# Kernel optimization log

Hardware: AMD Instinct MI355X
Metric: run time of the kernel (lower is better)

The kernel has to match this reference:

```python
import jax, jax.numpy as jnp
import numpy as np

NH = 2  # attention heads


def _mha(q, k, v, w, b, pool):
    """2-head attention; w:[4,D,D] (q,k,v,o as x@W), b:[4,D], pool:[Lq] pools query axis -> [B,D]."""
    B, Lq, D = q.shape
    dk = D // NH
    Q = (q @ w[0] + b[0]).reshape(B, Lq, NH, dk).transpose(0, 2, 1, 3)
    K = (k @ w[1] + b[1]).reshape(B, -1, NH, dk).transpose(0, 2, 1, 3)
    V = (v @ w[2] + b[2]).reshape(B, -1, NH, dk).transpose(0, 2, 1, 3)
    scores = jnp.einsum('bhqd,bhkd->bhqk', Q, K) / jnp.sqrt(jnp.asarray(dk, q.dtype))
    attn = jax.nn.softmax(scores, axis=-1)
    ctx = jnp.einsum('bhqk,bhkd->bqhd', attn, V).reshape(B, Lq, D)
    out = ctx @ w[3] + b[3]              # [B, Lq, D]
    return jnp.einsum('bqd,q->bd', out, pool)  # pooled over query axis (w_size)


def setup_inputs() -> dict:
    key = jax.random.key(0)
    ks = jax.random.split(key, 32)
    B, T, D, N = 64, 32, 768, 901
    s = 0.02
    inp = {
        'question_embeds': jax.random.normal(ks[0], (B, T, D), jnp.float32),
        'image_local_embeds': jax.random.normal(ks[1], (B, N, D), jnp.float32),
        'h0': jax.random.uniform(ks[2], (B, D), jnp.float32),
        'gru_w_ih': jax.random.normal(ks[3], (3 * D, D), jnp.float32) * s,
        'gru_w_hh': jax.random.normal(ks[4], (3 * D, D), jnp.float32) * s,
        'gru_b_ih': jax.random.normal(ks[5], (3 * D,), jnp.float32) * s,
        'gru_b_hh': jax.random.normal(ks[6], (3 * D,), jnp.float32) * s,
        'ga_w': jax.random.normal(ks[7], (4, D, D), jnp.float32) * s,
        'ga_b': jax.random.normal(ks[8], (4, D), jnp.float32) * s,
        'ga_pool': jax.random.normal(ks[9], (1,), jnp.float32),
        'la_w': jax.random.normal(ks[10], (4, D, D), jnp.float32) * s,
        'la_b': jax.random.normal(ks[11], (4, D), jnp.float32) * s,
        'la_pool': jax.random.normal(ks[12], (T,), jnp.float32) * 0.2,
        'go_w': jax.random.normal(ks[13], (4, D, D), jnp.float32) * s,
        'go_b': jax.random.normal(ks[14], (4, D), jnp.float32) * s,
        'go_pool': jax.random.normal(ks[15], (T,), jnp.float32) * 0.2,
        'f1_w': jax.random.normal(ks[16], (2 * D, 1024), jnp.float32) * s,
        'f1_b': jax.random.normal(ks[17], (1024,), jnp.float32) * s,
        'f2_w': jax.random.normal(ks[18], (1024, 512), jnp.float32) * s,
        'f2_b': jax.random.normal(ks[19], (512,), jnp.float32) * s,
        'f3_w': jax.random.normal(ks[20], (512, 1024), jnp.float32) * s,
        'f3_b': jax.random.normal(ks[21], (1024,), jnp.float32) * s,
    }
    return inp


def reference(question_embeds, image_local_embeds, h0,
              gru_w_ih, gru_w_hh, gru_b_ih, gru_b_hh,
              ga_w, ga_b, ga_pool, la_w, la_b, la_pool,
              go_w, go_b, go_pool,
              f1_w, f1_b, f2_w, f2_b, f3_w, f3_b):
    img_cls = image_local_embeds[:, :1, :]        # [B,1,D] global CLS token
    img_loc = image_local_embeds[:, 1:, :]        # [B,N-1,D] patch tokens
    Hs = h0.shape[-1]

    def step(h, x_t):
        # per-timestep cross-attention of question token against image CLS
        a = _mha(x_t[:, None, :], img_cls, img_cls, ga_w, ga_b, ga_pool)  # [B,D]
        wx = a @ gru_w_ih.T                      # [B,3H]
        wh = h @ gru_w_hh.T
        r = jax.nn.sigmoid(wx[:, :Hs] + wh[:, :Hs] + gru_b_ih[:Hs] + gru_b_hh[:Hs])
        z = jax.nn.sigmoid(wx[:, Hs:2 * Hs] + wh[:, Hs:2 * Hs]
                           + gru_b_ih[Hs:2 * Hs] + gru_b_hh[Hs:2 * Hs])
        n = jnp.tanh(wx[:, 2 * Hs:] + gru_b_ih[2 * Hs:]
                     + r * (wh[:, 2 * Hs:] + gru_b_hh[2 * Hs:]))
        h_new = (1 - z) * n + z * h
        return h_new, h_new

    xs = jnp.swapaxes(question_embeds, 0, 1)      # [T,B,D]
    _, ys = jax.lax.scan(step, h0, xs)
    q_emb = jnp.swapaxes(ys, 0, 1)                # [B,T,D]

    local_out = _mha(q_emb, img_loc, img_loc, la_w, la_b, la_pool)   # [B,D]
    gobal_out = _mha(q_emb, img_cls, img_cls, go_w, go_b, go_pool)   # [B,D]
    h = jnp.concatenate([local_out, gobal_out], axis=1)              # [B,2D]
    x = h @ f1_w + f1_b
    x = jax.nn.relu(x @ f2_w + f2_b)
    return x @ f3_w + f3_b                                           # [B,1024]
```

## Files before the change

### kernel.cpp

```cpp
#include <hip/hip_runtime.h>
#include <math.h>


typedef short bf16x8 __attribute__((ext_vector_type(8)));
typedef float f32x4 __attribute__((ext_vector_type(4)));
typedef unsigned short ushort_t;

#define GRU_NB 48

__device__ __forceinline__ unsigned short f2b(float f) {
    unsigned int u = __float_as_uint(f);
    unsigned int r = (u + 0x7FFFu + ((u >> 16) & 1u)) >> 16;
    return (unsigned short)r;
}
__device__ __forceinline__ float b2f(unsigned short s) {
    return __uint_as_float(((unsigned int)s) << 16);
}
__device__ __forceinline__ float sigm(float x) { return 1.f / (1.f + __expf(-x)); }
__device__ __forceinline__ float tanhx(float x) {
    x = fminf(fmaxf(x, -15.f), 15.f);
    float e = __expf(2.f * x);
    return (e - 1.f) / (e + 1.f);
}

__device__ __forceinline__ void gbar(int* flags, int nb, int phase, int bid, int tid) {
    __syncthreads();
    if (tid == 0) __hip_atomic_store(&flags[bid], phase, __ATOMIC_RELAXED, __HIP_MEMORY_SCOPE_AGENT);
    if (tid < 64) {
        for (;;) {
            int v = 0x7fffffff;
            for (int f = tid; f < nb; f += 64)
                v = min(v, __hip_atomic_load(&flags[f], __ATOMIC_RELAXED, __HIP_MEMORY_SCOPE_AGENT));
            if (__all(v >= phase)) break;
            __builtin_amdgcn_s_sleep(1);
        }
    }
    __syncthreads();
}


__global__ void k_cvt_all(const float* __restrict__ whh, const float* __restrict__ la0,
                          const float* __restrict__ la1, const float* __restrict__ h0,
                          const float* __restrict__ gp, const float* __restrict__ lp,
                          ushort_t* __restrict__ whhb, ushort_t* __restrict__ law0b,
                          ushort_t* __restrict__ law1b, ushort_t* __restrict__ h0b,
                          float* __restrict__ hbuf, float* __restrict__ scal,
                          int* __restrict__ bar) {
    if (blockIdx.x == 0) {
        int t = threadIdx.x;
        if (t < 64) {
            float v1 = (t < 32) ? gp[t] : 0.f;
            float v2 = (t < 32) ? lp[t] : 0.f;
#pragma unroll
            for (int m = 1; m < 32; m <<= 1) { v1 += __shfl_xor(v1, m, 64); v2 += __shfl_xor(v2, m, 64); }
            if (t == 0) { scal[0] = v1; scal[1] = v2; }
        }
        for (int i = threadIdx.x; i < 1024; i += 256) bar[i] = 0;
    }
    long i = (long)blockIdx.x * 256 + threadIdx.x;
    const long n1 = 2304L * 768, n2 = n1 + 768L * 768, n3 = n2 + 768L * 768, n4 = n3 + 64L * 768;
    if (i < n1) whhb[i] = f2b(whh[i]);
    else if (i < n2) law0b[i - n1] = f2b(la0[i - n1]);
    else if (i < n3) law1b[i - n2] = f2b(la1[i - n2]);
    else if (i < n4) { float v = h0[i - n3]; h0b[i - n3] = f2b(v); hbuf[i - n3] = v; }
}


template<int MR>
__device__ __forceinline__ void tgemm4(
    const float* __restrict__ A, long lda,
    const float* __restrict__ Bm, int ldb, int transB,
    const float* __restrict__ bias, float s1, float s2,
    const float* __restrict__ bias2, int b2lim,
    float* __restrict__ C, int ldc, int K, int relu, int agent,
    int m0, int n0, float* As, int tid)
{
    for (int r = 0; r < MR; r++)
        for (int k = tid; k < K; k += 256)
            As[r * K + k] = A[(long)(m0 + r) * lda + k];
    __syncthreads();
    int cl = tid & 63, kc = tid >> 6;
    int c = n0 + cl;
    int K4 = K >> 2;
    int kb = kc * K4;
    const float* Bp = transB ? (Bm + (long)c * ldb) : (Bm + c);
    float acc[MR];
#pragma unroll
    for (int r = 0; r < MR; r++) acc[r] = 0.f;
    for (int k = kb; k < kb + K4; k += 8) {
        float bv[8];
        if (!transB) {
#pragma unroll
            for (int i = 0; i < 8; i++) bv[i] = Bp[(long)(k + i) * ldb];
        } else {
            float4 q0 = *(const float4*)(Bp + k);
            float4 q1 = *(const float4*)(Bp + k + 4);
            bv[0] = q0.x; bv[1] = q0.y; bv[2] = q0.z; bv[3] = q0.w;
            bv[4] = q1.x; bv[5] = q1.y; bv[6] = q1.z; bv[7] = q1.w;
        }
#pragma unroll
        for (int i = 0; i < 8; i += 4) {
#pragma unroll
            for (int r = 0; r < MR; r++) {
                float4 x = *(const float4*)&As[r * K + k + i];
                acc[r] += x.x * bv[i] + x.y * bv[i + 1] + x.z * bv[i + 2] + x.w * bv[i + 3];
            }
        }
    }
    __syncthreads();
    float* Red = As;
#pragma unroll
    for (int r = 0; r < MR; r++) Red[(kc * MR + r) * 64 + cl] = acc[r];
    __syncthreads();
    {
        int rg = tid >> 6;
        float bb = (bias ? bias[c] * s2 : 0.f) + ((bias2 && c < b2lim) ? bias2[c] : 0.f);
#pragma unroll
        for (int i = 0; i < MR / 4; i++) {
            int r = rg + i * 4;
            float sum = (Red[(0 * MR + r) * 64 + cl] + Red[(1 * MR + r) * 64 + cl])
                      + (Red[(2 * MR + r) * 64 + cl] + Red[(3 * MR + r) * 64 + cl]);
            float o = sum * s1 + bb;
            if (relu) o = fmaxf(o, 0.f);
            if (agent) __hip_atomic_store(&C[(long)(m0 + r) * ldc + c], o,
                                          __ATOMIC_RELAXED, __HIP_MEMORY_SCOPE_AGENT);
            else C[(long)(m0 + r) * ldc + c] = o;
        }
    }
}


struct HeadP {
    const float *img, *ga_w2, *ga_b2, *go_w2, *go_b2;
    const float *ga_w3, *ga_b3, *go_w3, *go_b3;
    const float *ga_pool, *scal, *w_ih, *b_ih, *b_hh;
    float *t12, *t12g, *avec, *hcat, *base;
    int* flags; int p0, p1;
};

__global__ void __launch_bounds__(256) k_head(HeadP P) {
    __shared__ __align__(16) float As[16 * 768];
    int bid = blockIdx.x, tid = threadIdx.x;
    for (int p = P.p0; p <= P.p1; p++) {
        if (p == 1) {
            if (bid < 192) {
                int prob = bid / 96, r = bid % 96, m8 = r / 12, ct = r % 12;
                tgemm4<8>(P.img, 901L * 768, prob ? P.go_w2 : P.ga_w2, 768, 0,
                          prob ? P.go_b2 : P.ga_b2, 1.f, 1.f, nullptr, 0,
                          prob ? P.t12g : P.t12, 768, 768, 0, 1, m8 * 8, ct * 64, As, tid);
            }
        } else if (p == 2) {
            if (bid < 192) {
                int prob = bid / 96, r = bid % 96, m8 = r / 12, ct = r % 12;
                float sc = prob ? P.scal[0] : P.ga_pool[0];
                tgemm4<8>(prob ? P.t12g : P.t12, 768, prob ? P.go_w3 : P.ga_w3, 768, 0,
                          prob ? P.go_b3 : P.ga_b3, sc, sc, nullptr, 0,
                          prob ? (P.hcat + 768) : P.avec, prob ? 1536 : 768, 768, 0, 1,
                          m8 * 8, ct * 64, As, tid);
            }
        } else if (p == 3) {
            if (bid < 144) {
                int m4 = bid / 36, ct = bid % 36;
                tgemm4<16>(P.avec, 768, P.w_ih, 768, 1, P.b_ih, 1.f, 1.f, P.b_hh, 1536,
                           P.base, 2304, 768, 0, 0, m4 * 16, ct * 64, As, tid);
            }
        }
        if (p < P.p1) gbar(P.flags, 192, p, bid, tid);
    }
}


struct GruP {
    const ushort_t* h0b; const float* h0f; const ushort_t* whh;
    const float* base; const float* bhh; ushort_t* qemb; int* flags;
};

__global__ void __launch_bounds__(384) k_gru_coop(GruP P) {
    __shared__ __align__(16) ushort_t whh_s[3][16][776];
    __shared__ float ps[2][3][64][20];
    __shared__ float bs[3][64][20];
    __shared__ float h_s[64][20];
    __shared__ float bhh_s[16];
    int tid = threadIdx.x;
    int wid = tid >> 6, lane = tid & 63, quad = lane >> 4, l16 = lane & 15;
    int g = wid >> 1, kh = wid & 1;
    int j = blockIdx.x, d0 = j * 16;
    {
        int gS = (wid < 3) ? wid : wid - 3;
        int r0 = (wid < 3) ? 0 : 8;
        for (int r = r0; r < r0 + 8; r++)
            for (int kk = lane * 8; kk < 768; kk += 512)
                *(bf16x8*)&whh_s[gS][r][kk] = *(const bf16x8*)&P.whh[(size_t)(gS * 768 + d0 + r) * 768 + kk];
    }
    for (int e = tid; e < 3072; e += 384) {
        int g2 = e >> 10, rem = e & 1023, b = rem >> 4, c = rem & 15;
        bs[g2][b][c] = P.base[b * 2304 + g2 * 768 + d0 + c];
    }
    for (int e = tid; e < 1024; e += 384) {
        int b = e >> 4, c = e & 15;
        h_s[b][c] = P.h0f[b * 768 + d0 + c];
    }
    if (tid < 16) bhh_s[tid] = P.bhh[1536 + d0 + tid];
    __syncthreads();
    for (int t = 0; t < 32; t++) {
        const ushort_t* Ap = (t == 0) ? P.h0b : (P.qemb + (size_t)(t - 1) * 768);
        size_t ldA = (t == 0) ? 768 : (size_t)32 * 768;
        f32x4 zz4 = {0.f, 0.f, 0.f, 0.f};
        f32x4 acc[4];
#pragma unroll
        for (int mi = 0; mi < 4; mi++) acc[mi] = zz4;
        int kbase = kh * 384;
        for (int kk = kbase; kk < kbase + 384; kk += 32) {
            bf16x8 bfr = *(const bf16x8*)&whh_s[g][l16][kk + quad * 8];
#pragma unroll
            for (int mi = 0; mi < 4; mi++) {
                bf16x8 af = *(const bf16x8*)(Ap + (size_t)(mi * 16 + l16) * ldA + kk + quad * 8);
                acc[mi] = __builtin_amdgcn_mfma_f32_16x16x32_bf16(af, bfr, acc[mi], 0, 0, 0);
            }
        }
#pragma unroll
        for (int mi = 0; mi < 4; mi++)
#pragma unroll
            for (int r = 0; r < 4; r++)
                ps[kh][g][mi * 16 + quad * 4 + r][l16] = acc[mi][r];
        __syncthreads();
        for (int e = tid; e < 512; e += 384) {
            int b = e >> 3, c0 = (e & 7) * 2;
            float hn[2];
#pragma unroll
            for (int u = 0; u < 2; u++) {
                int c = c0 + u;
                float g0 = ps[0][0][b][c] + ps[1][0][b][c];
                float g1 = ps[0][1][b][c] + ps[1][1][b][c];
                float g2v = ps[0][2][b][c] + ps[1][2][b][c];
                float rr = sigm(g0 + bs[0][b][c]);
                float zg = sigm(g1 + bs[1][b][c]);
                float nn = tanhx(bs[2][b][c] + rr * (g2v + bhh_s[c]));
                float hv = h_s[b][c];
                hn[u] = (1.f - zg) * nn + zg * hv;
                h_s[b][c] = hn[u];
            }
            unsigned int pk = (unsigned int)f2b(hn[0]) | ((unsigned int)f2b(hn[1]) << 16);
            __hip_atomic_store((unsigned int*)&P.qemb[((size_t)b * 32 + t) * 768 + d0 + c0],
                               pk, __ATOMIC_RELAXED, __HIP_MEMORY_SCOPE_AGENT);
        }
        __syncthreads();
        if (t < 31) {
            if (tid == 0)
                __hip_atomic_store(&P.flags[j], t + 1, __ATOMIC_RELAXED, __HIP_MEMORY_SCOPE_AGENT);
            if (tid < 64) {
                for (;;) {
                    int v = (tid < GRU_NB)
                        ? __hip_atomic_load(&P.flags[tid], __ATOMIC_RELAXED, __HIP_MEMORY_SCOPE_AGENT)
                        : 0x7fffffff;
                    if (__all(v > t)) break;
                    __builtin_amdgcn_s_sleep(1);
                }
            }
            __syncthreads();
        }
    }
}

__global__ void __launch_bounds__(256) k_gru_step(
    int t, const ushort_t* h0b, const ushort_t* whh, const float* base,
    const float* bhh, float* h, ushort_t* qemb)
{
    int wv = threadIdx.x >> 6, lane = threadIdx.x & 63;
    int quad = lane >> 4, l16 = lane & 15;
    int d0 = blockIdx.x * 64 + wv * 16;
    float bhhn = bhh[1536 + d0 + l16];
    const ushort_t* Ap = (t == 0) ? h0b : (qemb + (long)(t - 1) * 768);
    long ldA = (t == 0) ? 768 : 32 * 768;
    int d = d0 + l16;
    f32x4 zz4 = {0.f, 0.f, 0.f, 0.f};
    f32x4 acc[3][4];
#pragma unroll
    for (int g = 0; g < 3; g++)
#pragma unroll
        for (int mi = 0; mi < 4; mi++) acc[g][mi] = zz4;
    for (int kk = 0; kk < 768; kk += 32) {
        bf16x8 af[4];
#pragma unroll
        for (int mi = 0; mi < 4; mi++)
            af[mi] = *(const bf16x8*)(Ap + (long)(mi * 16 + l16) * ldA + kk + quad * 8);
#pragma unroll
        for (int g = 0; g < 3; g++) {
            bf16x8 bfr = *(const bf16x8*)(whh + (long)(g * 768 + d0 + l16) * 768 + kk + quad * 8);
#pragma unroll
            for (int mi = 0; mi < 4; mi++)
                acc[g][mi] = __builtin_amdgcn_mfma_f32_16x16x32_bf16(af[mi], bfr, acc[g][mi], 0, 0, 0);
        }
    }
#pragma unroll
    for (int mi = 0; mi < 4; mi++) {
#pragma unroll
        for (int r = 0; r < 4; r++) {
            int b = mi * 16 + quad * 4 + r;
            const float* bb = base + b * 2304;
            float rr = sigm(acc[0][mi][r] + bb[d]);
            float zg = sigm(acc[1][mi][r] + bb[768 + d]);
            float nn = tanhx(bb[1536 + d] + rr * (acc[2][mi][r] + bhhn));
            float hv = h[b * 768 + d];
            float hnew = (1.f - zg) * nn + zg * hv;
            h[b * 768 + d] = hnew;
            qemb[(long)(b * 32 + t) * 768 + d] = f2b(hnew);
        }
    }
}


__global__ void __launch_bounds__(256) k_gemm_bf16(
    const ushort_t* __restrict__ A, int lda,
    const ushort_t* __restrict__ B, int ldb, int transB,
    const float* __restrict__ bias,
    ushort_t* __restrict__ Cb, int ldc,
    int K, int remap, int rowoff)
{
    __shared__ __align__(16) ushort_t As[64][72];
    __shared__ __align__(16) ushort_t Bs[64][72];
    int tid = threadIdx.x;
    int wv = tid >> 6, lane = tid & 63, quad = lane >> 4, l16 = lane & 15;
    long bm = (long)blockIdx.y * 64, bn = (long)blockIdx.x * 64;
    f32x4 zz4 = {0.f, 0.f, 0.f, 0.f};
    f32x4 acc[4];
#pragma unroll
    for (int mi = 0; mi < 4; mi++) acc[mi] = zz4;
    int row4 = tid >> 2, seg = tid & 3;
    for (int k0 = 0; k0 < K; k0 += 64) {
        {
            const ushort_t* src = A + (bm + row4) * lda + k0 + seg * 16;
            *(bf16x8*)&As[row4][seg * 16] = *(const bf16x8*)src;
            *(bf16x8*)&As[row4][seg * 16 + 8] = *(const bf16x8*)(src + 8);
        }
        if (transB) {
            const ushort_t* src = B + (bn + row4) * ldb + k0 + seg * 16;
            *(bf16x8*)&Bs[row4][seg * 16] = *(const bf16x8*)src;
            *(bf16x8*)&Bs[row4][seg * 16 + 8] = *(const bf16x8*)(src + 8);
        } else {
            const ushort_t* src = B + (long)(k0 + row4) * ldb + bn + seg * 16;
            bf16x8 v0 = *(const bf16x8*)src;
            bf16x8 v1 = *(const bf16x8*)(src + 8);
#pragma unroll
            for (int i = 0; i < 8; i++) {
                Bs[seg * 16 + i][row4] = (ushort_t)v0[i];
                Bs[seg * 16 + 8 + i][row4] = (ushort_t)v1[i];
            }
        }
        __syncthreads();
#pragma unroll
        for (int ks = 0; ks < 64; ks += 32) {
            bf16x8 bfr = *(const bf16x8*)&Bs[wv * 16 + l16][ks + quad * 8];
#pragma unroll
            for (int mi = 0; mi < 4; mi++) {
                bf16x8 af = *(const bf16x8*)&As[mi * 16 + l16][ks + quad * 8];
                acc[mi] = __builtin_amdgcn_mfma_f32_16x16x32_bf16(af, bfr, acc[mi], 0, 0, 0);
            }
        }
        __syncthreads();
    }
    int ncol = (int)bn + wv * 16 + l16;
    float bv = bias ? bias[ncol] : 0.f;
#pragma unroll
    for (int mi = 0; mi < 4; mi++) {
#pragma unroll
        for (int r = 0; r < 4; r++) {
            long row = bm + mi * 16 + quad * 4 + r;
            long orow = remap ? ((row >> 5) * 64 + rowoff + (row & 31)) : row;
            Cb[orow * ldc + ncol] = f2b(acc[mi][r] + bv);
        }
    }
}


__global__ void __launch_bounds__(512) k_flash(
    const float* __restrict__ img, const ushort_t* __restrict__ Qt,
    const ushort_t* __restrict__ Qb, const float* __restrict__ la_b1,
    float* __restrict__ pm, float* __restrict__ pl,
    ushort_t* __restrict__ pacc, int nsplit)
{
    __shared__ __align__(16) ushort_t xs[32][776];
    __shared__ float Sls[64][36];
    __shared__ __align__(16) ushort_t Pls[64][40];
    __shared__ float m_s[64], l_s[64], al_s[64], qb_s[64];
    int b = blockIdx.x;
    int sp = blockIdx.y;
    int tper = (29 + nsplit - 1) / nsplit;
    int tb = sp * tper, te = min(29, tb + tper);
    int tid = threadIdx.x;
    int wv = tid >> 6, lane = tid & 63, quad = lane >> 4, l16 = lane & 15;
    {
        int row = tid >> 3, sub = tid & 7;
        int hh = row >> 5, q = row & 31;
        const ushort_t* src = Qb + ((size_t)(b * 32 + q)) * 768 + hh * 384 + sub * 48;
        const float* bb = la_b1 + hh * 384 + sub * 48;
        float s = 0.f;
#pragma unroll
        for (int k = 0; k < 48; k++) s += b2f(src[k]) * bb[k];
        s += __shfl_xor(s, 1, 64); s += __shfl_xor(s, 2, 64); s += __shfl_xor(s, 4, 64);
        if (sub == 0) qb_s[row] = s;
    }
    if (tid < 64) { m_s[tid] = -1e30f; l_s[tid] = 0.f; }
    f32x4 zz4 = {0.f, 0.f, 0.f, 0.f};
    f32x4 acc[4][6];
#pragma unroll
    for (int mi = 0; mi < 4; mi++)
#pragma unroll
        for (int nj = 0; nj < 6; nj++) acc[mi][nj] = zz4;
    const float rs = 0.051031036307982884f;
    int smi = wv & 3, sni = wv >> 2;
    __syncthreads();
    for (int t0 = tb; t0 < te; t0++) {
        int key0 = t0 * 32;
        {
            int keyl = tid >> 4, dseg = tid & 15;
            int key = key0 + keyl;
            const float* src = img + ((long)b * 901 + 1 + key) * 768;
            bool ok = key < 900;
#pragma unroll
            for (int c = 0; c < 12; c++) {
                int dd = c * 64 + dseg * 4;
                float x0 = 0, x1 = 0, x2 = 0, x3 = 0;
                if (ok) { float4 v = *(const float4*)(src + dd); x0 = v.x; x1 = v.y; x2 = v.z; x3 = v.w; }
                ushort_t* dst = &xs[keyl][dd];
                dst[0] = f2b(x0); dst[1] = f2b(x1); dst[2] = f2b(x2); dst[3] = f2b(x3);
            }
        }
        __syncthreads();
        {
            f32x4 as = zz4;
            const ushort_t* qrow = Qt + (long)(b * 64 + smi * 16 + l16) * 768 + quad * 8;
            const ushort_t* xrow = &xs[sni * 16 + l16][quad * 8];
#pragma unroll
            for (int kk = 0; kk < 768; kk += 32) {
                bf16x8 aq = *(const bf16x8*)(qrow + kk);
                bf16x8 bx = *(const bf16x8*)(xrow + kk);
                as = __builtin_amdgcn_mfma_f32_16x16x32_bf16(aq, bx, as, 0, 0, 0);
            }
#pragma unroll
            for (int r = 0; r < 4; r++) {
                int row = smi * 16 + quad * 4 + r;
                Sls[row][sni * 16 + l16] = (as[r] + qb_s[row]) * rs;
            }
        }
        __syncthreads();
        {
            int row = tid >> 3, sub = tid & 7;
            float sv[4];
            float mx = -1e30f;
#pragma unroll
            for (int i = 0; i < 4; i++) {
                int kl = sub + i * 8;
                float s = (key0 + kl < 900) ? Sls[row][kl] : -1e30f;
                sv[i] = s; mx = fmaxf(mx, s);
            }
            mx = fmaxf(mx, __shfl_xor(mx, 1, 64));
            mx = fmaxf(mx, __shfl_xor(mx, 2, 64));
            mx = fmaxf(mx, __shfl_xor(mx, 4, 64));
            float mold = m_s[row];
            float mnew = fmaxf(mold, mx);
            float ss = 0.f;
#pragma unroll
            for (int i = 0; i < 4; i++) {
                float p = __expf(sv[i] - mnew);
                ss += p;
                Pls[row][sub + i * 8] = f2b(p);
            }
            ss += __shfl_xor(ss, 1, 64);
            ss += __shfl_xor(ss, 2, 64);
            ss += __shfl_xor(ss, 4, 64);
            if (sub == 0) {
                float alpha = __expf(mold - mnew);
                al_s[row] = alpha;
                l_s[row] = l_s[row] * alpha + ss;
                m_s[row] = mnew;
            }
        }
        __syncthreads();
        {
            bf16x8 pf[4];
#pragma unroll
            for (int mi = 0; mi < 4; mi++)
                pf[mi] = *(const bf16x8*)&Pls[mi * 16 + l16][quad * 8];
#pragma unroll
            for (int mi = 0; mi < 4; mi++) {
#pragma unroll
                for (int r = 0; r < 4; r++) {
                    float a = al_s[mi * 16 + quad * 4 + r];
#pragma unroll
                    for (int nj = 0; nj < 6; nj++) acc[mi][nj][r] *= a;
                }
            }
#pragma unroll
            for (int nj = 0; nj < 6; nj++) {
                int dd = wv * 96 + nj * 16 + l16;
                bf16x8 bx;
#pragma unroll
                for (int j = 0; j < 8; j++) bx[j] = (short)xs[quad * 8 + j][dd];
#pragma unroll
                for (int mi = 0; mi < 4; mi++)
                    acc[mi][nj] = __builtin_amdgcn_mfma_f32_16x16x32_bf16(pf[mi], bx, acc[mi][nj], 0, 0, 0);
            }
        }
        __syncthreads();
    }
    if (tid < 64) {
        pm[(b * nsplit + sp) * 64 + tid] = m_s[tid];
        pl[(b * nsplit + sp) * 64 + tid] = l_s[tid];
    }
#pragma unroll
    for (int mi = 0; mi < 4; mi++) {
#pragma unroll
        for (int r = 0; r < 4; r++) {
            int row = mi * 16 + quad * 4 + r;
            ushort_t* dst = pacc + ((size_t)(b * nsplit + sp) * 64 + row) * 768;
#pragma unroll
            for (int nj = 0; nj < 6; nj++)
                dst[wv * 96 + nj * 16 + l16] = f2b(acc[mi][nj][r]);
        }
    }
}


struct TailP {
    const float *pm, *pl; const ushort_t* pacc; const float* lp;
    const float *la_w2, *la_b2, *la_w3, *la_b3, *scal;
    float *plX, *pc, *hcat;
    const float *f1w, *f1b, *f2w, *f2b, *f3w, *f3b;
    float *x1, *x2, *out;
    int* flags; int p0, p1, nsplit;
};

template<int NS>
__global__ void __launch_bounds__(256) k_tail(TailP P) {
    __shared__ __align__(16) float As[4 * 1536];
    __shared__ float cw[NS][64];
    int bid = blockIdx.x, tid = threadIdx.x;
    float sla = P.scal[1];
    for (int p = P.p0; p <= P.p1; p++) {
        if (p == 0) {
            if (bid < 192) {
                int b = bid / 3, jj = bid % 3;
                if (tid < 64) {
                    int row = tid;
                    float ex[NS];
                    float mmax = -1e30f;
#pragma unroll
                    for (int s = 0; s < NS; s++) mmax = fmaxf(mmax, P.pm[(b * NS + s) * 64 + row]);
                    float lsum = 0.f;
#pragma unroll
                    for (int s = 0; s < NS; s++) {
                        ex[s] = __expf(P.pm[(b * NS + s) * 64 + row] - mmax);
                        lsum += ex[s] * P.pl[(b * NS + s) * 64 + row];
                    }
                    float sc = P.lp[row & 31] / lsum;
#pragma unroll
                    for (int s = 0; s < NS; s++) cw[s][row] = ex[s] * sc;
                }
                __syncthreads();
                int col = jj * 256 + tid;
                const ushort_t* pp = P.pacc + ((size_t)(b * NS)) * 64 * 768 + col;
                float ac0 = 0.f, ac1 = 0.f;
                for (int q = 0; q < 32; q += 2) {
                    float vv[2][NS][2];
#pragma unroll
                    for (int u = 0; u < 2; u++)
#pragma unroll
                        for (int s = 0; s < NS; s++) {
                            vv[u][s][0] = b2f(pp[((size_t)(s * 64 + q + u)) * 768]);
                            vv[u][s][1] = b2f(pp[((size_t)(s * 64 + 32 + q + u)) * 768]);
                        }
#pragma unroll
                    for (int u = 0; u < 2; u++)
#pragma unroll
                        for (int s = 0; s < NS; s++) {
                            ac0 += cw[s][q + u] * vv[u][s][0];
                            ac1 += cw[s][32 + q + u] * vv[u][s][1];
                        }
                }
                __hip_atomic_store(&P.plX[b * 1536 + col], ac0,
                                   __ATOMIC_RELAXED, __HIP_MEMORY_SCOPE_AGENT);
                __hip_atomic_store(&P.plX[b * 1536 + 768 + col], ac1,
                                   __ATOMIC_RELAXED, __HIP_MEMORY_SCOPE_AGENT);
            }
        } else if (p == 1) {
            if (bid < 192) {
                int m4 = bid / 12, ct = bid % 12, prob = ct / 6;
                tgemm4<4>(P.plX + prob * 768, 1536, P.la_w2, 768, 0,
                          P.la_b2, 1.f, sla, nullptr, 0,
                          P.pc, 768, 768, 0, 1, m4 * 4, ct * 64, As, tid);
            }
        } else if (p == 2) {
            if (bid < 192) {
                int m4 = bid / 12, ct = bid % 12;
                tgemm4<4>(P.pc, 768, P.la_w3, 768, 0, P.la_b3, 1.f, sla, nullptr, 0,
                          P.hcat, 1536, 768, 0, 1, m4 * 4, ct * 64, As, tid);
            }
        } else if (p == 3) {
            if (bid < 256) {
                int m4 = bid / 16, ct = bid % 16;
                tgemm4<4>(P.hcat, 1536, P.f1w, 1024, 0, P.f1b, 1.f, 1.f, nullptr, 0,
                          P.x1, 1024, 1536, 0, 1, m4 * 4, ct * 64, As, tid);
            }
        } else if (p == 4) {
            if (bid < 128) {
                int m4 = bid / 8, ct = bid % 8;
                tgemm4<4>(P.x1, 1024, P.f2w, 512, 0, P.f2b, 1.f, 1.f, nullptr, 0,
                          P.x2, 512, 1024, 1, 1, m4 * 4, ct * 64, As, tid);
            }
        } else if (p == 5) {
            if (bid < 256) {
                int m4 = bid / 16, ct = bid % 16;
                tgemm4<4>(P.x2, 512, P.f3w, 1024, 0, P.f3b, 1.f, 1.f, nullptr, 0,
                          P.out, 1024, 512, 0, 0, m4 * 4, ct * 64, As, tid);
            }
        }
        if (p < P.p1) gbar(P.flags, 256, p + 1, bid, tid);
    }
}


extern "C" void kernel_launch(void* const* d_in, const int* in_sizes, int n_in,
                              void* d_out, int out_size, void* d_ws, size_t ws_size,
                              hipStream_t stream)
{
    const float* img  = (const float*)d_in[1];
    const float* h0   = (const float*)d_in[2];
    const float* w_ih = (const float*)d_in[3];
    const float* w_hh = (const float*)d_in[4];
    const float* b_ih = (const float*)d_in[5];
    const float* b_hh = (const float*)d_in[6];
    const float* ga_w = (const float*)d_in[7];
    const float* ga_b = (const float*)d_in[8];
    const float* ga_pool = (const float*)d_in[9];
    const float* la_w = (const float*)d_in[10];
    const float* la_b = (const float*)d_in[11];
    const float* la_pool = (const float*)d_in[12];
    const float* go_w = (const float*)d_in[13];
    const float* go_b = (const float*)d_in[14];
    const float* go_pool = (const float*)d_in[15];
    const float* f1w = (const float*)d_in[16];
    const float* f1b = (const float*)d_in[17];
    const float* f2w = (const float*)d_in[18];
    const float* f2b_ = (const float*)d_in[19];
    const float* f3w = (const float*)d_in[20];
    const float* f3b = (const float*)d_in[21];
    float* out = (float*)d_out;
    (void)in_sizes; (void)n_in; (void)out_size;

    int nsplit = (ws_size >= (size_t)43 * 1024 * 1024) ? 4 : 2;

    char* w = (char*)d_ws;
    auto alloc = [&](size_t bytes) -> char* {
        char* p = w; w += (bytes + 255) & ~(size_t)255; return p;
    };
    float*    scal  = (float*)alloc(256);
    int*      bar   = (int*)alloc(4096);
    ushort_t* law0b = (ushort_t*)alloc((size_t)768 * 768 * 2);
    ushort_t* law1b = (ushort_t*)alloc((size_t)768 * 768 * 2);
    ushort_t* h0b   = (ushort_t*)alloc((size_t)64 * 768 * 2);
    ushort_t* qembb = (ushort_t*)alloc((size_t)2048 * 768 * 2);
    ushort_t* Qb    = (ushort_t*)alloc((size_t)2048 * 768 * 2);
    ushort_t* Qtb   = (ushort_t*)alloc((size_t)4096 * 768 * 2);
    float*    pm    = (float*)alloc((size_t)64 * 4 * 64 * 4);
    float*    pl    = (float*)alloc((size_t)64 * 4 * 64 * 4);
    float*    plX   = (float*)alloc((size_t)64 * 1536 * 4);
    float*    pc    = (float*)alloc((size_t)64 * 768 * 4);
    float*    hcat  = (float*)alloc((size_t)64 * 1536 * 4);
    float*    x1    = (float*)alloc((size_t)64 * 1024 * 4);
    float*    x2    = (float*)alloc((size_t)64 * 512 * 4);
    char* uni = w;
    char* u = uni;
    auto ualloc = [&](size_t bytes) -> char* {
        char* p = u; u += (bytes + 255) & ~(size_t)255; return p;
    };
    ushort_t* whhb  = (ushort_t*)ualloc((size_t)2304 * 768 * 2);
    float*    t12   = (float*)ualloc((size_t)2 * 64 * 768 * 4);
    float*    avec  = (float*)ualloc((size_t)64 * 768 * 4);
    float*    base  = (float*)ualloc((size_t)64 * 2304 * 4);
    float*    hbuf  = (float*)ualloc((size_t)64 * 768 * 4);
    ushort_t* pacc  = (ushort_t*)uni;
    float*    t12g  = t12 + 64 * 768;

    const float* ga_w2 = ga_w + 2 * 768 * 768; const float* ga_w3 = ga_w + 3 * 768 * 768;
    const float* ga_b2 = ga_b + 2 * 768;       const float* ga_b3 = ga_b + 3 * 768;
    const float* go_w2 = go_w + 2 * 768 * 768; const float* go_w3 = go_w + 3 * 768 * 768;
    const float* go_b2 = go_b + 2 * 768;       const float* go_b3 = go_b + 3 * 768;
    const float* la_w0 = la_w;                 const float* la_w1 = la_w + 768 * 768;
    const float* la_w2 = la_w + 2 * 768 * 768; const float* la_w3 = la_w + 3 * 768 * 768;
    const float* la_b0 = la_b;                 const float* la_b1 = la_b + 768;
    const float* la_b2 = la_b + 2 * 768;       const float* la_b3 = la_b + 3 * 768;

    dim3 blk(256);
    k_cvt_all<<<11712, blk, 0, stream>>>(w_hh, la_w0, la_w1, h0, go_pool, la_pool,
                                         whhb, law0b, law1b, h0b, hbuf, scal, bar);

    {
        HeadP P;
        P.img = img; P.ga_w2 = ga_w2; P.ga_b2 = ga_b2; P.go_w2 = go_w2; P.go_b2 = go_b2;
        P.ga_w3 = ga_w3; P.ga_b3 = ga_b3; P.go_w3 = go_w3; P.go_b3 = go_b3;
        P.ga_pool = ga_pool; P.scal = scal; P.w_ih = w_ih; P.b_ih = b_ih; P.b_hh = b_hh;
        P.t12 = t12; P.t12g = t12g; P.avec = avec; P.hcat = hcat; P.base = base;
        P.flags = bar + 64; P.p0 = 1; P.p1 = 3;
        void* args[1] = { &P };
        hipError_t e = hipLaunchCooperativeKernel((void*)k_head, dim3(192), blk, args, 0, stream);
        if (e != hipSuccess)
            for (int p = 1; p <= 3; p++) { P.p0 = P.p1 = p; k_head<<<192, blk, 0, stream>>>(P); }
    }

    {
        GruP P;
        P.h0b = h0b; P.h0f = h0; P.whh = whhb; P.base = base; P.bhh = b_hh;
        P.qemb = qembb; P.flags = bar;
        void* args[1] = { &P };
        hipError_t e = hipLaunchCooperativeKernel((void*)k_gru_coop, dim3(GRU_NB), dim3(384),
                                                  args, 0, stream);
        if (e != hipSuccess)
            for (int t = 0; t < 32; t++)
                k_gru_step<<<12, blk, 0, stream>>>(t, h0b, whhb, base, b_hh, hbuf, qembb);
    }

    k_gemm_bf16<<<dim3(12, 32), blk, 0, stream>>>(qembb, 768, law0b, 768, 0, la_b0, Qb, 768, 768, 0, 0);
    k_gemm_bf16<<<dim3(12, 32), blk, 0, stream>>>(Qb, 768, law1b, 768, 1, nullptr, Qtb, 768, 384, 1, 0);
    k_gemm_bf16<<<dim3(12, 32), blk, 0, stream>>>(Qb + 384, 768, law1b + 384, 768, 1, nullptr, Qtb, 768, 384, 1, 32);

    k_flash<<<dim3(64, nsplit), dim3(512), 0, stream>>>(img, Qtb, Qb, la_b1, pm, pl, pacc, nsplit);

    {
        TailP P;
        P.pm = pm; P.pl = pl; P.pacc = pacc; P.lp = la_pool;
        P.la_w2 = la_w2; P.la_b2 = la_b2; P.la_w3 = la_w3; P.la_b3 = la_b3; P.scal = scal;
        P.plX = plX; P.pc = pc; P.hcat = hcat;
        P.f1w = f1w; P.f1b = f1b; P.f2w = f2w; P.f2b = f2b_; P.f3w = f3w; P.f3b = f3b;
        P.x1 = x1; P.x2 = x2; P.out = out;
        P.flags = bar + 320; P.p0 = 0; P.p1 = 5; P.nsplit = nsplit;
        void* args[1] = { &P };
        if (nsplit == 4) {
            hipError_t e = hipLaunchCooperativeKernel((void*)k_tail<4>, dim3(256), blk, args, 0, stream);
            if (e != hipSuccess)
                for (int p = 0; p <= 5; p++) { P.p0 = P.p1 = p; k_tail<4><<<256, blk, 0, stream>>>(P); }
        } else {
            hipError_t e = hipLaunchCooperativeKernel((void*)k_tail<2>, dim3(256), blk, args, 0, stream);
            if (e != hipSuccess)
                for (int p = 0; p <= 5; p++) { P.p0 = P.p1 = p; k_tail<2><<<256, blk, 0, stream>>>(P); }
        }
    }
}
```

Baseline: 1.138 ms.

## Stage GRU hidden-state tiles in LDS and split MFMA work by batch rows

Each GRU timestep now loads the previous hidden state cooperatively into shared memory in four K-chunks of 192, instead of every wave reading its A fragments straight from global memory. The waves now split the batch rows (mh) rather than the K dimension, so the cross-wave partial-sum reduction goes away and the result buffer reuses the staging space. The goal is to cut redundant global and L2 reads on the latency-bound recurrent path. The cost is extra __syncthreads barriers per chunk and per step.

```diff
diff --git a/kernel.cpp b/kernel.cpp
--- a/kernel.cpp
+++ b/kernel.cpp
@@ -177,13 +177,14 @@
 
 __global__ void __launch_bounds__(384) k_gru_coop(GruP P) {
     __shared__ __align__(16) ushort_t whh_s[3][16][776];
-    __shared__ float ps[2][3][64][20];
+    __shared__ __align__(16) ushort_t as_s[64][200];
     __shared__ float bs[3][64][20];
     __shared__ float h_s[64][20];
     __shared__ float bhh_s[16];
+    float* gs = (float*)&as_s[0][0];
     int tid = threadIdx.x;
     int wid = tid >> 6, lane = tid & 63, quad = lane >> 4, l16 = lane & 15;
-    int g = wid >> 1, kh = wid & 1;
+    int g = wid >> 1, mh = wid & 1;
     int j = blockIdx.x, d0 = j * 16;
     {
         int gS = (wid < 3) ? wid : wid - 3;
@@ -206,23 +207,33 @@
         const ushort_t* Ap = (t == 0) ? P.h0b : (P.qemb + (size_t)(t - 1) * 768);
         size_t ldA = (t == 0) ? 768 : (size_t)32 * 768;
         f32x4 zz4 = {0.f, 0.f, 0.f, 0.f};
-        f32x4 acc[4];
-#pragma unroll
-        for (int mi = 0; mi < 4; mi++) acc[mi] = zz4;
-        int kbase = kh * 384;
-        for (int kk = kbase; kk < kbase + 384; kk += 32) {
-            bf16x8 bfr = *(const bf16x8*)&whh_s[g][l16][kk + quad * 8];
-#pragma unroll
-            for (int mi = 0; mi < 4; mi++) {
-                bf16x8 af = *(const bf16x8*)(Ap + (size_t)(mi * 16 + l16) * ldA + kk + quad * 8);
-                acc[mi] = __builtin_amdgcn_mfma_f32_16x16x32_bf16(af, bfr, acc[mi], 0, 0, 0);
-            }
-        }
-#pragma unroll
-        for (int mi = 0; mi < 4; mi++)
+        f32x4 acc[2];
+        acc[0] = zz4; acc[1] = zz4;
+        for (int kq = 0; kq < 4; kq++) {
+            __syncthreads();
+#pragma unroll
+            for (int i = 0; i < 4; i++) {
+                int id = i * 384 + tid;
+                int row = id / 24, c = id % 24;
+                *(bf16x8*)&as_s[row][c * 8] =
+                    *(const bf16x8*)(Ap + (size_t)row * ldA + kq * 192 + c * 8);
+            }
+            __syncthreads();
+            for (int kk = 0; kk < 192; kk += 32) {
+                bf16x8 bfr = *(const bf16x8*)&whh_s[g][l16][kq * 192 + kk + quad * 8];
+#pragma unroll
+                for (int mi = 0; mi < 2; mi++) {
+                    bf16x8 af = *(const bf16x8*)&as_s[mh * 32 + mi * 16 + l16][kk + quad * 8];
+                    acc[mi] = __builtin_amdgcn_mfma_f32_16x16x32_bf16(af, bfr, acc[mi], 0, 0, 0);
+                }
+            }
+        }
+        __syncthreads();
+#pragma unroll
+        for (int mi = 0; mi < 2; mi++)
 #pragma unroll
             for (int r = 0; r < 4; r++)
-                ps[kh][g][mi * 16 + quad * 4 + r][l16] = acc[mi][r];
+                gs[((size_t)g * 64 + mh * 32 + mi * 16 + quad * 4 + r) * 20 + l16] = acc[mi][r];
         __syncthreads();
         for (int e = tid; e < 512; e += 384) {
             int b = e >> 3, c0 = (e & 7) * 2;
@@ -230,9 +241,9 @@
 #pragma unroll
             for (int u = 0; u < 2; u++) {
                 int c = c0 + u;
-                float g0 = ps[0][0][b][c] + ps[1][0][b][c];
-                float g1 = ps[0][1][b][c] + ps[1][1][b][c];
-                float g2v = ps[0][2][b][c] + ps[1][2][b][c];
+                float g0 = gs[((size_t)0 * 64 + b) * 20 + c];
+                float g1 = gs[((size_t)1 * 64 + b) * 20 + c];
+                float g2v = gs[((size_t)2 * 64 + b) * 20 + c];
                 float rr = sigm(g0 + bs[0][b][c]);
                 float zg = sigm(g1 + bs[1][b][c]);
                 float nn = tanhx(bs[2][b][c] + rr * (g2v + bhh_s[c]));
```

Measured after the change: 1.006 ms. 1.13x faster.
